# Performance work log

Measured on AMD Instinct MI355X. Metric: run time of the kernel, lower is better.

Reference implementation:

```python
import jax, jax.numpy as jnp
import numpy as np

B, T = 64, 20          # batch, caption length
C, HW = 512, 196       # cnn_channels, width*height (14x14)
V, E, U = 10000, 256, 512  # n_tokens, emb_size, lstm_units
MAX_NORM = 5.0


def setup_inputs() -> dict:
    key = jax.random.key(0)
    ks = jax.random.split(key, 12)
    s = 0.02
    return {
        "image_features": jax.random.normal(ks[0], (B, C, HW), jnp.float32),
        "captions_ix": jax.random.randint(ks[1], (B, T), 0, V, dtype=jnp.int32),
        "W_h0": jax.random.normal(ks[2], (U, C), jnp.float32) * s,
        "b_h0": jnp.zeros((U,), jnp.float32),
        "W_c0": jax.random.normal(ks[3], (U, C), jnp.float32) * s,
        "b_c0": jnp.zeros((U,), jnp.float32),
        "emb": jax.random.normal(ks[4], (V, E), jnp.float32) * s,
        "W_key": jax.random.normal(ks[5], (U, C), jnp.float32) * s,
        "b_key": jnp.zeros((U,), jnp.float32),
        "W_ih": jax.random.normal(ks[6], (4 * U, C + E), jnp.float32) * s,
        "b_ih": jnp.zeros((4 * U,), jnp.float32),
        "W_hh": jax.random.normal(ks[7], (4 * U, U), jnp.float32) * s,
        "b_hh": jnp.zeros((4 * U,), jnp.float32),
        "W_out": jax.random.normal(ks[8], (V, C + E + U), jnp.float32) * s,
        "b_out": jnp.zeros((V,), jnp.float32),
    }


def _caption_net(image_features, captions_ix, W_h0, b_h0, W_c0, b_c0, emb,
                 W_key, b_key, W_ih, b_ih, W_hh, b_hh, W_out, b_out):
    feats_mean = image_features.mean(axis=2)                # [B, C]
    hid0 = feats_mean @ W_h0.T + b_h0                       # [B, U]
    cell0 = feats_mean @ W_c0.T + b_c0                      # [B, U]
    feats = jnp.transpose(image_features, (0, 2, 1))        # [B, HW, C]
    keys = feats @ W_key.T + b_key                          # [B, HW, U]

    # nn.Embedding(max_norm=5): renorm rows whose L2 norm exceeds 5
    norms = jnp.linalg.norm(emb, axis=1, keepdims=True)
    emb_eff = emb * jnp.minimum(1.0, MAX_NORM / jnp.maximum(norms, 1e-12))
    cap_emb = emb_eff[captions_ix]                          # [B, T, E]

    inv_scale = 1.0 / (keys.shape[2] ** 0.5)

    def step(carry, emb_t):
        hid, cell = carry
        # scaled dot-product attention, query = current hidden state
        scores = jnp.einsum('bu,bku->bk', hid, keys) * inv_scale   # [B, HW]
        w = jax.nn.softmax(scores, axis=1)
        a = jnp.einsum('bk,bkc->bc', w, feats)                     # [B, C]
        x = jnp.concatenate([emb_t, a], axis=1)                    # [B, E+C]
        gates = x @ W_ih.T + b_ih + hid @ W_hh.T + b_hh            # [B, 4U]
        i, f, g, o = jnp.split(gates, 4, axis=1)
        cell = jax.nn.sigmoid(f) * cell + jax.nn.sigmoid(i) * jnp.tanh(g)
        hid = jax.nn.sigmoid(o) * jnp.tanh(cell)
        out = jnp.concatenate([hid, a, emb_t], axis=1)             # [B, U+C+E]
        return (hid, cell), (out, w)

    (_, _), (outs, attn) = jax.lax.scan(step, (hid0, cell0),
                                        jnp.transpose(cap_emb, (1, 0, 2)))
    outs = jnp.transpose(outs, (1, 0, 2))                   # [B, T, U+C+E]
    attn = jnp.transpose(attn, (1, 0, 2))                   # [B, T, HW]
    logits = outs @ W_out.T + b_out                         # [B, T, V]
    return logits, attn


def reference(image_features, captions_ix, W_h0, b_h0, W_c0, b_c0, emb,
              W_key, b_key, W_ih, b_ih, W_hh, b_hh, W_out, b_out):
    return _caption_net(image_features, captions_ix, W_h0, b_h0, W_c0, b_c0,
                        emb, W_key, b_key, W_ih, b_ih, W_hh, b_hh, W_out, b_out)
```

## Files before the change

kernel.cpp:

```cpp
#include <hip/hip_runtime.h>
#include <math.h>

#define B 64
#define T 20
#define C 512
#define HW 196
#define V 10000
#define E 256
#define U 512
#define G4U 2048
#define ODIM 1280
#define KTOT 1280

typedef short bf8_t __attribute__((ext_vector_type(8)));
typedef float f4_t  __attribute__((ext_vector_type(4)));

__device__ __forceinline__ unsigned short f2bf(float f) {
    unsigned int u = __float_as_uint(f);
    return (unsigned short)((u + 0x7fffu + ((u >> 16) & 1u)) >> 16);
}
__device__ __forceinline__ float bf2f(unsigned short s) {
    return __uint_as_float((unsigned int)s << 16);
}
__device__ __forceinline__ float bflo(unsigned int kv) { return __uint_as_float(kv << 16); }
__device__ __forceinline__ float bfhi(unsigned int kv) { return __uint_as_float(kv & 0xffff0000u); }

__global__ void k_mean(const float* __restrict__ img, float* __restrict__ fm) {
    int wave = threadIdx.x >> 6;
    int lane = threadIdx.x & 63;
    int row = blockIdx.x * 4 + wave;
    const float* p = img + (size_t)row * HW;
    float s = p[lane] + p[lane + 64] + p[lane + 128];
    if (lane < 4) s += p[lane + 192];
    for (int off = 32; off > 0; off >>= 1) s += __shfl_down(s, off, 64);
    if (lane == 0) fm[row] = s * (1.0f / HW);
}

__global__ void k_init(const float* __restrict__ fm,
                       const float* __restrict__ W_h0, const float* __restrict__ b_h0,
                       const float* __restrict__ W_c0, const float* __restrict__ b_c0,
                       unsigned short* __restrict__ xb, float* __restrict__ cell) {
    int wv = blockIdx.x * 4 + (threadIdx.x >> 6);
    int lane = threadIdx.x & 63;
    int which = wv >> 15;
    int r = wv & 32767;
    int b = r >> 9, u = r & 511;
    const float* W = which ? W_c0 : W_h0;
    const float* bias = which ? b_c0 : b_h0;
    const float* f = fm + b * C;
    const float* w = W + (size_t)u * C;
    float s = 0.f;
    #pragma unroll
    for (int c = 0; c < C; c += 64) s += f[c + lane] * w[c + lane];
    for (int off = 32; off > 0; off >>= 1) s += __shfl_down(s, off, 64);
    if (lane == 0) {
        float v = s + bias[u];
        if (which) cell[r] = v;
        else       xb[(size_t)b * KTOT + 768 + u] = f2bf(v);
    }
}

__global__ void k_wkt(const float* __restrict__ Wk, float* __restrict__ WkT) {
    __shared__ float tile[64][65];
    int u0 = blockIdx.x * 64, c0 = blockIdx.y * 64;
    int x = threadIdx.x & 63, y0 = threadIdx.x >> 6;
    #pragma unroll
    for (int i = 0; i < 16; i++) {
        int r = y0 * 16 + i;
        tile[r][x] = Wk[(size_t)(u0 + r) * C + c0 + x];
    }
    __syncthreads();
    #pragma unroll
    for (int i = 0; i < 16; i++) {
        int r = y0 * 16 + i;
        WkT[(size_t)(c0 + r) * U + u0 + x] = tile[x][r];
    }
}

__global__ __launch_bounds__(256) void k_keys(const float* __restrict__ img,
        const float* __restrict__ WkT, const float* __restrict__ b_key,
        unsigned short* __restrict__ keys2) {
    __shared__ unsigned short st[32][200];
    int b = blockIdx.x >> 4;
    int u0 = (blockIdx.x & 15) * 32;
    int wave = __builtin_amdgcn_readfirstlane(threadIdx.x >> 6);
    int lane = threadIdx.x & 63;
    int lk = lane < 49 ? lane : 48;
    const f4_t* imgb = (const f4_t*)(img + (size_t)b * C * HW);
    f4_t acc[8];
    #pragma unroll
    for (int j = 0; j < 8; j++) acc[j] = (f4_t){0.f, 0.f, 0.f, 0.f};
    const float* wp = WkT + u0 + wave * 8;
    for (int c = 0; c < C; c++) {
        f4_t v = imgb[c * 49 + lk];
        const float* w = wp + (size_t)c * U;
        #pragma unroll
        for (int j = 0; j < 8; j++) acc[j] += v * w[j];
    }
    if (lane < 49) {
        #pragma unroll
        for (int j = 0; j < 8; j++) {
            float bk = b_key[u0 + wave * 8 + j];
            int ul = wave * 8 + j;
            int k = lane * 4;
            st[ul][k + 0] = f2bf(acc[j].x + bk);
            st[ul][k + 1] = f2bf(acc[j].y + bk);
            st[ul][k + 2] = f2bf(acc[j].z + bk);
            st[ul][k + 3] = f2bf(acc[j].w + bk);
        }
    }
    __syncthreads();
    int ui = threadIdx.x & 15;
    int kr = threadIdx.x >> 4;
    #pragma unroll
    for (int pass = 0; pass < 13; pass++) {
        int k = pass * 16 + kr;
        if (k < HW) {
            unsigned int lo = st[ui * 2][k];
            unsigned int hi = st[ui * 2 + 1][k];
            *(unsigned int*)&keys2[((size_t)b * HW + k) * U + u0 + ui * 2] = (hi << 16) | lo;
        }
    }
}

__global__ void k_wg(const float* __restrict__ W_ih, const float* __restrict__ W_hh,
                     unsigned short* __restrict__ Wg) {
    int j = blockIdx.x;
    int tid = threadIdx.x;
    const float* s1 = W_ih + (size_t)j * 768;
    const float* s2 = W_hh + (size_t)j * 512;
    unsigned short* dst = Wg + (size_t)j * KTOT;
    #pragma unroll
    for (int p = 0; p < 3; p++) dst[tid + p * 256] = f2bf(s1[tid + p * 256]);
    #pragma unroll
    for (int p = 0; p < 2; p++) dst[768 + tid + p * 256] = f2bf(s2[tid + p * 256]);
}

__global__ void k_emb(const int* __restrict__ ix, const float* __restrict__ emb,
                      unsigned short* __restrict__ outs) {
    int bt = blockIdx.x;
    int e = threadIdx.x;
    int row = ix[bt];
    float v = emb[(size_t)row * E + e];
    __shared__ float red[4];
    float sq = v * v;
    for (int off = 32; off > 0; off >>= 1) sq += __shfl_down(sq, off, 64);
    int wave = e >> 6, lane = e & 63;
    if (lane == 0) red[wave] = sq;
    __syncthreads();
    float norm = sqrtf(red[0] + red[1] + red[2] + red[3]);
    float scale = fminf(1.0f, 5.0f / fmaxf(norm, 1e-12f));
    outs[(size_t)bt * ODIM + (U + C) + e] = f2bf(v * scale);
}

__global__ __launch_bounds__(256) void k_step(
    unsigned short* __restrict__ outs, unsigned short* __restrict__ xb,
    float* __restrict__ cell, const float* __restrict__ gates_buf,
    const unsigned short* __restrict__ keys2, const float* __restrict__ img,
    const float* __restrict__ b_ih, const float* __restrict__ b_hh,
    float* __restrict__ attn, int t) {
    int b = blockIdx.x;
    int tid = threadIdx.x;
    int wave = tid >> 6, lane = tid & 63;
    __shared__ float hidS[U];
    __shared__ float wS[256];
    __shared__ float red[4];

    if (t > 0) {
        #pragma unroll
        for (int p = 0; p < 2; p++) {
            int u = tid + p * 256;
            float g[4];
            #pragma unroll
            for (int q = 0; q < 4; q++) {
                int j = q * 512 + u;
                g[q] = gates_buf[(size_t)b * G4U + j] + b_ih[j] + b_hh[j];
            }
            float si = 1.f / (1.f + expf(-g[0]));
            float sf = 1.f / (1.f + expf(-g[1]));
            float tg = tanhf(g[2]);
            float so = 1.f / (1.f + expf(-g[3]));
            int ci = b * U + u;
            float cn = sf * cell[ci] + si * tg;
            float hn = so * tanhf(cn);
            cell[ci] = cn;
            hidS[u] = hn;
            outs[((size_t)b * T + (t - 1)) * ODIM + u] = f2bf(hn);
            xb[(size_t)b * KTOT + 768 + u] = f2bf(hn);
        }
    } else {
        #pragma unroll
        for (int p = 0; p < 2; p++) {
            int u = tid + p * 256;
            hidS[u] = bf2f(xb[(size_t)b * KTOT + 768 + u]);
        }
    }
    if (t >= T) return;
    __syncthreads();

    float sc = 0.f;
    if (tid < HW) {
        const uint4* kr = (const uint4*)(keys2 + ((size_t)b * HW + tid) * U);
        float acc = 0.f;
        #pragma unroll 8
        for (int i = 0; i < 64; i++) {
            uint4 kv = kr[i];
            float4 h0 = *(const float4*)&hidS[i * 8];
            float4 h1 = *(const float4*)&hidS[i * 8 + 4];
            acc += bflo(kv.x) * h0.x + bfhi(kv.x) * h0.y
                 + bflo(kv.y) * h0.z + bfhi(kv.y) * h0.w
                 + bflo(kv.z) * h1.x + bfhi(kv.z) * h1.y
                 + bflo(kv.w) * h1.z + bfhi(kv.w) * h1.w;
        }
        sc = acc * 0.044194173824159216f;
    }
    {
        float v = (tid < HW) ? sc : -1e30f;
        float m = v;
        for (int off = 32; off > 0; off >>= 1) m = fmaxf(m, __shfl_down(m, off, 64));
        if (lane == 0) red[wave] = m;
        __syncthreads();
        m = fmaxf(fmaxf(red[0], red[1]), fmaxf(red[2], red[3]));
        float ex = (tid < HW) ? expf(v - m) : 0.f;
        float ssum = ex;
        for (int off = 32; off > 0; off >>= 1) ssum += __shfl_down(ssum, off, 64);
        __syncthreads();
        if (lane == 0) red[wave] = ssum;
        __syncthreads();
        ssum = red[0] + red[1] + red[2] + red[3];
        float w = ex / ssum;
        wS[tid] = w;
        if (tid < HW) attn[((size_t)b * T + t) * HW + tid] = w;
    }
    __syncthreads();

    {
        const float4* imgb = (const float4*)(img + (size_t)b * C * HW);
        #pragma unroll
        for (int p = 0; p < 2; p++) {
            int c = tid + p * 256;
            const float4* r = imgb + c * 49;
            float acc = 0.f;
            for (int k4 = 0; k4 < 49; k4++) {
                float4 vv = r[k4];
                acc += wS[4 * k4] * vv.x + wS[4 * k4 + 1] * vv.y
                     + wS[4 * k4 + 2] * vv.z + wS[4 * k4 + 3] * vv.w;
            }
            xb[(size_t)b * KTOT + 256 + c] = f2bf(acc);
            outs[((size_t)b * T + t) * ODIM + U + c] = f2bf(acc);
        }
    }
    if (tid < 128) {
        const unsigned int* src = (const unsigned int*)(outs + ((size_t)b * T + t) * ODIM);
        unsigned int* dst = (unsigned int*)(xb + (size_t)b * KTOT);
        dst[tid] = src[512 + tid];
    }
}

__global__ __launch_bounds__(256) void k_gates5(
    const unsigned short* __restrict__ xb, const unsigned short* __restrict__ Wg,
    float* __restrict__ gates_buf) {
    __shared__ unsigned short As[64][72];
    __shared__ unsigned short Bs[64][72];
    int j0 = blockIdx.x * 64;
    int tid = threadIdx.x;
    int lane = tid & 63;
    int wv = __builtin_amdgcn_readfirstlane(tid >> 6);
    int m16 = lane & 15, quad = lane >> 4;
    int r = tid >> 2;
    int kq = tid & 3;

    f4_t acc[4];
    #pragma unroll
    for (int i = 0; i < 4; i++) acc[i] = (f4_t){0.f, 0.f, 0.f, 0.f};

    for (int k0 = 0; k0 < KTOT; k0 += 64) {
        const uint4* ap = (const uint4*)&xb[(size_t)r * KTOT + k0 + kq * 16];
        uint4 a0 = ap[0], a1 = ap[1];
        const uint4* bp = (const uint4*)&Wg[(size_t)(j0 + r) * KTOT + k0 + kq * 16];
        uint4 b0 = bp[0], b1 = bp[1];
        *(uint4*)&As[r][kq * 16] = a0;
        *(uint4*)&As[r][kq * 16 + 8] = a1;
        *(uint4*)&Bs[r][kq * 16] = b0;
        *(uint4*)&Bs[r][kq * 16 + 8] = b1;
        __syncthreads();
        #pragma unroll
        for (int h = 0; h < 2; h++) {
            bf8_t bfr = *(const bf8_t*)&Bs[wv * 16 + m16][h * 32 + quad * 8];
            #pragma unroll
            for (int i = 0; i < 4; i++) {
                bf8_t afr = *(const bf8_t*)&As[i * 16 + m16][h * 32 + quad * 8];
                acc[i] = __builtin_amdgcn_mfma_f32_16x16x32_bf16(afr, bfr, acc[i], 0, 0, 0);
            }
        }
        __syncthreads();
    }
    int n = j0 + wv * 16 + m16;
    #pragma unroll
    for (int i = 0; i < 4; i++) {
        int mb = i * 16 + quad * 4;
        #pragma unroll
        for (int rr = 0; rr < 4; rr++)
            gates_buf[(size_t)(mb + rr) * G4U + n] = acc[i][rr];
    }
}

__global__ __launch_bounds__(256) void k_logits4(
    const unsigned short* __restrict__ A, const float* __restrict__ Wo,
    const float* __restrict__ bo, float* __restrict__ Cout) {
    __shared__ unsigned short As[128][72];
    __shared__ unsigned short Bs[128][72];
    int n0 = blockIdx.x * 128;
    int m0 = blockIdx.y * 128;
    int tid = threadIdx.x;
    int lane = tid & 63, wv = tid >> 6;
    int mw = (wv >> 1) * 64, nw = (wv & 1) * 64;
    int m16 = lane & 15, quad = lane >> 4;
    int srow = tid >> 1, shalf = tid & 1;

    f4_t acc[4][4];
    #pragma unroll
    for (int i = 0; i < 4; i++)
        #pragma unroll
        for (int j = 0; j < 4; j++)
            acc[i][j] = (f4_t){0.f, 0.f, 0.f, 0.f};

    for (int k0 = 0; k0 < KTOT; k0 += 64) {
        {
            const uint4* ap = (const uint4*)&A[(size_t)(m0 + srow) * KTOT + k0 + shalf * 32];
            uint4 a0 = ap[0], a1 = ap[1], a2 = ap[2], a3 = ap[3];
            uint4* dst = (uint4*)&As[srow][shalf * 32];
            dst[0] = a0; dst[1] = a1; dst[2] = a2; dst[3] = a3;
        }
        {
            int n = n0 + srow;
            uint4 q[4];
            if (n < V) {
                const float4* bp = (const float4*)&Wo[(size_t)n * KTOT + k0 + shalf * 32];
                #pragma unroll
                for (int g = 0; g < 4; g++) {
                    float4 f0 = bp[g * 2], f1 = bp[g * 2 + 1];
                    q[g].x = ((unsigned int)f2bf(f0.y) << 16) | f2bf(f0.x);
                    q[g].y = ((unsigned int)f2bf(f0.w) << 16) | f2bf(f0.z);
                    q[g].z = ((unsigned int)f2bf(f1.y) << 16) | f2bf(f1.x);
                    q[g].w = ((unsigned int)f2bf(f1.w) << 16) | f2bf(f1.z);
                }
            } else {
                #pragma unroll
                for (int g = 0; g < 4; g++) q[g] = (uint4){0u, 0u, 0u, 0u};
            }
            uint4* dst = (uint4*)&Bs[srow][shalf * 32];
            #pragma unroll
            for (int g = 0; g < 4; g++) dst[g] = q[g];
        }
        __syncthreads();
        #pragma unroll
        for (int h = 0; h < 2; h++) {
            bf8_t af[4], bf[4];
            #pragma unroll
            for (int i = 0; i < 4; i++)
                af[i] = *(const bf8_t*)&As[mw + i * 16 + m16][h * 32 + quad * 8];
            #pragma unroll
            for (int j = 0; j < 4; j++)
                bf[j] = *(const bf8_t*)&Bs[nw + j * 16 + m16][h * 32 + quad * 8];
            #pragma unroll
            for (int i = 0; i < 4; i++)
                #pragma unroll
                for (int j = 0; j < 4; j++)
                    acc[i][j] = __builtin_amdgcn_mfma_f32_16x16x32_bf16(af[i], bf[j], acc[i][j], 0, 0, 0);
        }
        __syncthreads();
    }

    #pragma unroll
    for (int j = 0; j < 4; j++) {
        int n = n0 + nw + j * 16 + m16;
        if (n >= V) continue;
        float bias = bo[n];
        #pragma unroll
        for (int i = 0; i < 4; i++) {
            int mb = m0 + mw + i * 16 + quad * 4;
            #pragma unroll
            for (int r = 0; r < 4; r++)
                Cout[(size_t)(mb + r) * V + n] = acc[i][j][r] + bias;
        }
    }
}

extern "C" void kernel_launch(void* const* d_in, const int* in_sizes, int n_in,
                              void* d_out, int out_size, void* d_ws, size_t ws_size,
                              hipStream_t stream) {
    const float* img   = (const float*)d_in[0];
    const int*   capix = (const int*)d_in[1];
    const float* W_h0  = (const float*)d_in[2];
    const float* b_h0  = (const float*)d_in[3];
    const float* W_c0  = (const float*)d_in[4];
    const float* b_c0  = (const float*)d_in[5];
    const float* emb   = (const float*)d_in[6];
    const float* W_key = (const float*)d_in[7];
    const float* b_key = (const float*)d_in[8];
    const float* W_ih  = (const float*)d_in[9];
    const float* b_ih  = (const float*)d_in[10];
    const float* W_hh  = (const float*)d_in[11];
    const float* b_hh  = (const float*)d_in[12];
    const float* W_out = (const float*)d_in[13];
    const float* b_out = (const float*)d_in[14];

    float* ws = (float*)d_ws;
    float* gates_buf = ws;
    float* fm        = ws;
    float* cell      = gates_buf + 131072;
    float* WkT       = cell + 32768;
    unsigned short* Wg    = (unsigned short*)(WkT + 262144);
    unsigned short* xb    = Wg + 2621440;
    unsigned short* outs  = xb + 81920;
    unsigned short* keys2 = outs + (size_t)B * T * ODIM;

    float* logits = (float*)d_out;
    float* attn   = logits + (size_t)B * T * V;

    k_mean<<<(B * C) / 4, 256, 0, stream>>>(img, fm);
    k_init<<<(2 * B * U) / 4, 256, 0, stream>>>(fm, W_h0, b_h0, W_c0, b_c0, xb, cell);
    k_wkt<<<dim3(8, 8), 256, 0, stream>>>(W_key, WkT);
    k_keys<<<B * 16, 256, 0, stream>>>(img, WkT, b_key, keys2);
    k_wg<<<G4U, 256, 0, stream>>>(W_ih, W_hh, Wg);
    k_emb<<<B * T, 256, 0, stream>>>(capix, emb, outs);

    for (int t = 0; t < T; t++) {
        k_step<<<B, 256, 0, stream>>>(outs, xb, cell, gates_buf, keys2, img,
                                      b_ih, b_hh, attn, t);
        k_gates5<<<32, 256, 0, stream>>>(xb, Wg, gates_buf);
    }
    k_step<<<B, 256, 0, stream>>>(outs, xb, cell, gates_buf, keys2, img,
                                  b_ih, b_hh, attn, T);

    k_logits4<<<dim3((V + 127) / 128, (B * T) / 128), 256, 0, stream>>>(outs, W_out, b_out, logits);
}
```

Baseline: 1.381 ms.

## Fuse recurrent loop into one persistent kernel with grid barriers; pre-convert W_out

Replaces the 41 per-timestep launches (step + gates GEMM) with one persistent 64-block kernel that alternates attention/LSTM work and a split gates GEMM, separated by atomic-counter grid barriers; the cell state and bias sums are held in registers. It also adds a prefetching double-load in the gates GEMM and a separate pass converting W_out to bf16 once so the logits GEMM loads bf16 directly. This removes launch overhead and redundant fp32->bf16 conversion, at the risk of spin-barrier cost and co-residency assumptions for the 64 blocks.

```diff
diff --git a/kernel.cpp b/kernel.cpp
--- a/kernel.cpp
+++ b/kernel.cpp
@@ -11,6 +11,7 @@
 #define G4U 2048
 #define ODIM 1280
 #define KTOT 1280
+#define NBLK 64
 
 typedef short bf8_t __attribute__((ext_vector_type(8)));
 typedef float f4_t  __attribute__((ext_vector_type(4)));
@@ -25,7 +26,26 @@
 __device__ __forceinline__ float bflo(unsigned int kv) { return __uint_as_float(kv << 16); }
 __device__ __forceinline__ float bfhi(unsigned int kv) { return __uint_as_float(kv & 0xffff0000u); }
 
-__global__ void k_mean(const float* __restrict__ img, float* __restrict__ fm) {
+__device__ __forceinline__ void gbar(int* bar) {
+    __syncthreads();
+    if (threadIdx.x == 0) {
+        __threadfence();
+        int g = __hip_atomic_load(bar + 1, __ATOMIC_RELAXED, __HIP_MEMORY_SCOPE_AGENT);
+        if (__hip_atomic_fetch_add(bar, 1, __ATOMIC_RELAXED, __HIP_MEMORY_SCOPE_AGENT) == NBLK - 1) {
+            __hip_atomic_store(bar, 0, __ATOMIC_RELAXED, __HIP_MEMORY_SCOPE_AGENT);
+            __hip_atomic_store(bar + 1, g + 1, __ATOMIC_RELEASE, __HIP_MEMORY_SCOPE_AGENT);
+        } else {
+            while (__hip_atomic_load(bar + 1, __ATOMIC_RELAXED, __HIP_MEMORY_SCOPE_AGENT) == g)
+                __builtin_amdgcn_s_sleep(1);
+        }
+        __threadfence();
+    }
+    __syncthreads();
+}
+
+__global__ void k_mean(const float* __restrict__ img, float* __restrict__ fm,
+                       int* __restrict__ bar) {
+    if (blockIdx.x == 0 && threadIdx.x == 0) { bar[0] = 0; bar[1] = 0; }
     int wave = threadIdx.x >> 6;
     int lane = threadIdx.x & 63;
     int row = blockIdx.x * 4 + wave;
@@ -153,155 +173,181 @@
     outs[(size_t)bt * ODIM + (U + C) + e] = f2bf(v * scale);
 }
 
-__global__ __launch_bounds__(256) void k_step(
+__global__ __launch_bounds__(256) void k_wo(const float* __restrict__ W,
+                                            unsigned short* __restrict__ Wb) {
+    size_t i = ((size_t)blockIdx.x * 256 + threadIdx.x) * 8;
+    float4 f0 = *(const float4*)(W + i);
+    float4 f1 = *(const float4*)(W + i + 4);
+    uint4 q;
+    q.x = ((unsigned int)f2bf(f0.y) << 16) | f2bf(f0.x);
+    q.y = ((unsigned int)f2bf(f0.w) << 16) | f2bf(f0.z);
+    q.z = ((unsigned int)f2bf(f1.y) << 16) | f2bf(f1.x);
+    q.w = ((unsigned int)f2bf(f1.w) << 16) | f2bf(f1.z);
+    *(uint4*)(Wb + i) = q;
+}
+
+__global__ __launch_bounds__(256) void k_loop(
     unsigned short* __restrict__ outs, unsigned short* __restrict__ xb,
-    float* __restrict__ cell, const float* __restrict__ gates_buf,
+    const float* __restrict__ cell0, float* __restrict__ gates_buf,
     const unsigned short* __restrict__ keys2, const float* __restrict__ img,
     const float* __restrict__ b_ih, const float* __restrict__ b_hh,
-    float* __restrict__ attn, int t) {
+    const unsigned short* __restrict__ Wg, float* __restrict__ attn,
+    int* __restrict__ bar) {
     int b = blockIdx.x;
     int tid = threadIdx.x;
-    int wave = tid >> 6, lane = tid & 63;
+    int wave = __builtin_amdgcn_readfirstlane(tid >> 6);
+    int lane = tid & 63;
+    int m16 = lane & 15, quad = lane >> 4;
     __shared__ float hidS[U];
     __shared__ float wS[256];
     __shared__ float red[4];
-
-    if (t > 0) {
-        #pragma unroll
-        for (int p = 0; p < 2; p++) {
-            int u = tid + p * 256;
-            float g[4];
-            #pragma unroll
-            for (int q = 0; q < 4; q++) {
-                int j = q * 512 + u;
-                g[q] = gates_buf[(size_t)b * G4U + j] + b_ih[j] + b_hh[j];
-            }
-            float si = 1.f / (1.f + expf(-g[0]));
-            float sf = 1.f / (1.f + expf(-g[1]));
-            float tg = tanhf(g[2]);
-            float so = 1.f / (1.f + expf(-g[3]));
-            int ci = b * U + u;
-            float cn = sf * cell[ci] + si * tg;
-            float hn = so * tanhf(cn);
-            cell[ci] = cn;
-            hidS[u] = hn;
-            outs[((size_t)b * T + (t - 1)) * ODIM + u] = f2bf(hn);
-            xb[(size_t)b * KTOT + 768 + u] = f2bf(hn);
-        }
-    } else {
-        #pragma unroll
-        for (int p = 0; p < 2; p++) {
-            int u = tid + p * 256;
-            hidS[u] = bf2f(xb[(size_t)b * KTOT + 768 + u]);
-        }
-    }
-    if (t >= T) return;
-    __syncthreads();
-
-    float sc = 0.f;
-    if (tid < HW) {
-        const uint4* kr = (const uint4*)(keys2 + ((size_t)b * HW + tid) * U);
-        float acc = 0.f;
-        #pragma unroll 8
-        for (int i = 0; i < 64; i++) {
-            uint4 kv = kr[i];
-            float4 h0 = *(const float4*)&hidS[i * 8];
-            float4 h1 = *(const float4*)&hidS[i * 8 + 4];
-            acc += bflo(kv.x) * h0.x + bfhi(kv.x) * h0.y
-                 + bflo(kv.y) * h0.z + bfhi(kv.y) * h0.w
-                 + bflo(kv.z) * h1.x + bfhi(kv.z) * h1.y
-                 + bflo(kv.w) * h1.z + bfhi(kv.w) * h1.w;
-        }
-        sc = acc * 0.044194173824159216f;
-    }
-    {
-        float v = (tid < HW) ? sc : -1e30f;
-        float m = v;
-        for (int off = 32; off > 0; off >>= 1) m = fmaxf(m, __shfl_down(m, off, 64));
-        if (lane == 0) red[wave] = m;
+    __shared__ unsigned short As2[64][72];
+    __shared__ unsigned short Bs2[32][72];
+
+    float c_r[2], bsum[2][4];
+    #pragma unroll
+    for (int p = 0; p < 2; p++) {
+        int u = tid + p * 256;
+        c_r[p] = cell0[(size_t)b * U + u];
+        #pragma unroll
+        for (int q = 0; q < 4; q++)
+            bsum[p][q] = b_ih[q * 512 + u] + b_hh[q * 512 + u];
+    }
+
+    int j0g = blockIdx.x * 32;
+    int r = tid >> 2, kq = tid & 3;
+    int rb = tid >> 3, kb = tid & 7;
+    int n16 = wave & 1, mpair = wave >> 1;
+
+    for (int t = 0; t <= T; ++t) {
+        if (t > 0) {
+            #pragma unroll
+            for (int p = 0; p < 2; p++) {
+                int u = tid + p * 256;
+                float g[4];
+                #pragma unroll
+                for (int q = 0; q < 4; q++)
+                    g[q] = gates_buf[(size_t)b * G4U + q * 512 + u] + bsum[p][q];
+                float si = 1.f / (1.f + expf(-g[0]));
+                float sf = 1.f / (1.f + expf(-g[1]));
+                float tg = tanhf(g[2]);
+                float so = 1.f / (1.f + expf(-g[3]));
+                float cn = sf * c_r[p] + si * tg;
+                c_r[p] = cn;
+                float hn = so * tanhf(cn);
+                hidS[u] = hn;
+                outs[((size_t)b * T + (t - 1)) * ODIM + u] = f2bf(hn);
+                xb[(size_t)b * KTOT + 768 + u] = f2bf(hn);
+            }
+        } else {
+            #pragma unroll
+            for (int p = 0; p < 2; p++) {
+                int u = tid + p * 256;
+                hidS[u] = bf2f(xb[(size_t)b * KTOT + 768 + u]);
+            }
+        }
+        if (t == T) break;
         __syncthreads();
-        m = fmaxf(fmaxf(red[0], red[1]), fmaxf(red[2], red[3]));
-        float ex = (tid < HW) ? expf(v - m) : 0.f;
-        float ssum = ex;
-        for (int off = 32; off > 0; off >>= 1) ssum += __shfl_down(ssum, off, 64);
+
+        float sc = 0.f;
+        if (tid < HW) {
+            const uint4* kr = (const uint4*)(keys2 + ((size_t)b * HW + tid) * U);
+            float acc = 0.f;
+            #pragma unroll 8
+            for (int i = 0; i < 64; i++) {
+                uint4 kv = kr[i];
+                float4 h0 = *(const float4*)&hidS[i * 8];
+                float4 h1 = *(const float4*)&hidS[i * 8 + 4];
+                acc += bflo(kv.x) * h0.x + bfhi(kv.x) * h0.y
+                     + bflo(kv.y) * h0.z + bfhi(kv.y) * h0.w
+                     + bflo(kv.z) * h1.x + bfhi(kv.z) * h1.y
+                     + bflo(kv.w) * h1.z + bfhi(kv.w) * h1.w;
+            }
+            sc = acc * 0.044194173824159216f;
+        }
+        {
+            float v = (tid < HW) ? sc : -1e30f;
+            float m = v;
+            for (int off = 32; off > 0; off >>= 1) m = fmaxf(m, __shfl_down(m, off, 64));
+            if (lane == 0) red[wave] = m;
+            __syncthreads();
+            m = fmaxf(fmaxf(red[0], red[1]), fmaxf(red[2], red[3]));
+            float ex = (tid < HW) ? expf(v - m) : 0.f;
+            float ssum = ex;
+            for (int off = 32; off > 0; off >>= 1) ssum += __shfl_down(ssum, off, 64);
+            __syncthreads();
+            if (lane == 0) red[wave] = ssum;
+            __syncthreads();
+            ssum = red[0] + red[1] + red[2] + red[3];
+            float w = ex / ssum;
+            wS[tid] = w;
+            if (tid < HW) attn[((size_t)b * T + t) * HW + tid] = w;
+        }
         __syncthreads();
-        if (lane == 0) red[wave] = ssum;
-        __syncthreads();
-        ssum = red[0] + red[1] + red[2] + red[3];
-        float w = ex / ssum;
-        wS[tid] = w;
-        if (tid < HW) attn[((size_t)b * T + t) * HW + tid] = w;
-    }
-    __syncthreads();
-
-    {
-        const float4* imgb = (const float4*)(img + (size_t)b * C * HW);
-        #pragma unroll
-        for (int p = 0; p < 2; p++) {
-            int c = tid + p * 256;
-            const float4* r = imgb + c * 49;
-            float acc = 0.f;
-            for (int k4 = 0; k4 < 49; k4++) {
-                float4 vv = r[k4];
-                acc += wS[4 * k4] * vv.x + wS[4 * k4 + 1] * vv.y
-                     + wS[4 * k4 + 2] * vv.z + wS[4 * k4 + 3] * vv.w;
-            }
-            xb[(size_t)b * KTOT + 256 + c] = f2bf(acc);
-            outs[((size_t)b * T + t) * ODIM + U + c] = f2bf(acc);
-        }
-    }
-    if (tid < 128) {
-        const unsigned int* src = (const unsigned int*)(outs + ((size_t)b * T + t) * ODIM);
-        unsigned int* dst = (unsigned int*)(xb + (size_t)b * KTOT);
-        dst[tid] = src[512 + tid];
-    }
-}
-
-__global__ __launch_bounds__(256) void k_gates5(
-    const unsigned short* __restrict__ xb, const unsigned short* __restrict__ Wg,
-    float* __restrict__ gates_buf) {
-    __shared__ unsigned short As[64][72];
-    __shared__ unsigned short Bs[64][72];
-    int j0 = blockIdx.x * 64;
-    int tid = threadIdx.x;
-    int lane = tid & 63;
-    int wv = __builtin_amdgcn_readfirstlane(tid >> 6);
-    int m16 = lane & 15, quad = lane >> 4;
-    int r = tid >> 2;
-    int kq = tid & 3;
-
-    f4_t acc[4];
-    #pragma unroll
-    for (int i = 0; i < 4; i++) acc[i] = (f4_t){0.f, 0.f, 0.f, 0.f};
-
-    for (int k0 = 0; k0 < KTOT; k0 += 64) {
-        const uint4* ap = (const uint4*)&xb[(size_t)r * KTOT + k0 + kq * 16];
-        uint4 a0 = ap[0], a1 = ap[1];
-        const uint4* bp = (const uint4*)&Wg[(size_t)(j0 + r) * KTOT + k0 + kq * 16];
-        uint4 b0 = bp[0], b1 = bp[1];
-        *(uint4*)&As[r][kq * 16] = a0;
-        *(uint4*)&As[r][kq * 16 + 8] = a1;
-        *(uint4*)&Bs[r][kq * 16] = b0;
-        *(uint4*)&Bs[r][kq * 16 + 8] = b1;
-        __syncthreads();
-        #pragma unroll
-        for (int h = 0; h < 2; h++) {
-            bf8_t bfr = *(const bf8_t*)&Bs[wv * 16 + m16][h * 32 + quad * 8];
-            #pragma unroll
-            for (int i = 0; i < 4; i++) {
-                bf8_t afr = *(const bf8_t*)&As[i * 16 + m16][h * 32 + quad * 8];
-                acc[i] = __builtin_amdgcn_mfma_f32_16x16x32_bf16(afr, bfr, acc[i], 0, 0, 0);
-            }
-        }
-        __syncthreads();
-    }
-    int n = j0 + wv * 16 + m16;
-    #pragma unroll
-    for (int i = 0; i < 4; i++) {
-        int mb = i * 16 + quad * 4;
-        #pragma unroll
-        for (int rr = 0; rr < 4; rr++)
-            gates_buf[(size_t)(mb + rr) * G4U + n] = acc[i][rr];
+
+        {
+            const float4* imgb = (const float4*)(img + (size_t)b * C * HW);
+            #pragma unroll
+            for (int p = 0; p < 2; p++) {
+                int c = tid + p * 256;
+                const float4* rr4 = imgb + c * 49;
+                float acc = 0.f;
+                for (int k4 = 0; k4 < 49; k4++) {
+                    float4 vv = rr4[k4];
+                    acc += wS[4 * k4] * vv.x + wS[4 * k4 + 1] * vv.y
+                         + wS[4 * k4 + 2] * vv.z + wS[4 * k4 + 3] * vv.w;
+                }
+                xb[(size_t)b * KTOT + 256 + c] = f2bf(acc);
+                outs[((size_t)b * T + t) * ODIM + U + c] = f2bf(acc);
+            }
+        }
+        if (tid < 128) {
+            const unsigned int* src = (const unsigned int*)(outs + ((size_t)b * T + t) * ODIM);
+            unsigned int* dst = (unsigned int*)(xb + (size_t)b * KTOT);
+            dst[tid] = src[512 + tid];
+        }
+
+        gbar(bar);
+
+        {
+            f4_t acc2[2];
+            acc2[0] = (f4_t){0.f, 0.f, 0.f, 0.f};
+            acc2[1] = (f4_t){0.f, 0.f, 0.f, 0.f};
+            const uint4* ap0 = (const uint4*)&xb[(size_t)r * KTOT + kq * 16];
+            uint4 a0 = ap0[0], a1 = ap0[1];
+            uint4 bq = *(const uint4*)&Wg[(size_t)(j0g + rb) * KTOT + kb * 8];
+            for (int k0 = 0; k0 < KTOT; k0 += 64) {
+                *(uint4*)&As2[r][kq * 16]     = a0;
+                *(uint4*)&As2[r][kq * 16 + 8] = a1;
+                *(uint4*)&Bs2[rb][kb * 8]     = bq;
+                __syncthreads();
+                if (k0 + 64 < KTOT) {
+                    const uint4* apn = (const uint4*)&xb[(size_t)r * KTOT + k0 + 64 + kq * 16];
+                    a0 = apn[0]; a1 = apn[1];
+                    bq = *(const uint4*)&Wg[(size_t)(j0g + rb) * KTOT + k0 + 64 + kb * 8];
+                }
+                #pragma unroll
+                for (int h = 0; h < 2; h++) {
+                    bf8_t bfr = *(const bf8_t*)&Bs2[n16 * 16 + m16][h * 32 + quad * 8];
+                    #pragma unroll
+                    for (int i2 = 0; i2 < 2; i2++) {
+                        bf8_t afr = *(const bf8_t*)&As2[(mpair * 2 + i2) * 16 + m16][h * 32 + quad * 8];
+                        acc2[i2] = __builtin_amdgcn_mfma_f32_16x16x32_bf16(afr, bfr, acc2[i2], 0, 0, 0);
+                    }
+                }
+                __syncthreads();
+            }
+            int n = j0g + n16 * 16 + m16;
+            #pragma unroll
+            for (int i2 = 0; i2 < 2; i2++) {
+                int mb = (mpair * 2 + i2) * 16 + quad * 4;
+                #pragma unroll
+                for (int rr = 0; rr < 4; rr++)
+                    gates_buf[(size_t)(mb + rr) * G4U + n] = acc2[i2][rr];
+            }
+        }
+
+        gbar(bar);
     }
 }
 
@@ -345,6 +391,82 @@
                     q[g].z = ((unsigned int)f2bf(f1.y) << 16) | f2bf(f1.x);
                     q[g].w = ((unsigned int)f2bf(f1.w) << 16) | f2bf(f1.z);
                 }
+            } else {
+                #pragma unroll
+                for (int g = 0; g < 4; g++) q[g] = (uint4){0u, 0u, 0u, 0u};
+            }
+            uint4* dst = (uint4*)&Bs[srow][shalf * 32];
+            #pragma unroll
+            for (int g = 0; g < 4; g++) dst[g] = q[g];
+        }
+        __syncthreads();
+        #pragma unroll
+        for (int h = 0; h < 2; h++) {
+            bf8_t af[4], bf[4];
+            #pragma unroll
+            for (int i = 0; i < 4; i++)
+                af[i] = *(const bf8_t*)&As[mw + i * 16 + m16][h * 32 + quad * 8];
+            #pragma unroll
+            for (int j = 0; j < 4; j++)
+                bf[j] = *(const bf8_t*)&Bs[nw + j * 16 + m16][h * 32 + quad * 8];
+            #pragma unroll
+            for (int i = 0; i < 4; i++)
+                #pragma unroll
+                for (int j = 0; j < 4; j++)
+                    acc[i][j] = __builtin_amdgcn_mfma_f32_16x16x32_bf16(af[i], bf[j], acc[i][j], 0, 0, 0);
+        }
+        __syncthreads();
+    }
+
+    #pragma unroll
+    for (int j = 0; j < 4; j++) {
+        int n = n0 + nw + j * 16 + m16;
+        if (n >= V) continue;
+        float bias = bo[n];
+        #pragma unroll
+        for (int i = 0; i < 4; i++) {
+            int mb = m0 + mw + i * 16 + quad * 4;
+            #pragma unroll
+            for (int r = 0; r < 4; r++)
+                Cout[(size_t)(mb + r) * V + n] = acc[i][j][r] + bias;
+        }
+    }
+}
+
+__global__ __launch_bounds__(256) void k_logits5(
+    const unsigned short* __restrict__ A, const unsigned short* __restrict__ Wob,
+    const float* __restrict__ bo, float* __restrict__ Cout) {
+    __shared__ unsigned short As[128][72];
+    __shared__ unsigned short Bs[128][72];
+    int n0 = blockIdx.x * 128;
+    int m0 = blockIdx.y * 128;
+    int tid = threadIdx.x;
+    int lane = tid & 63, wv = tid >> 6;
+    int mw = (wv >> 1) * 64, nw = (wv & 1) * 64;
+    int m16 = lane & 15, quad = lane >> 4;
+    int srow = tid >> 1, shalf = tid & 1;
+
+    f4_t acc[4][4];
+    #pragma unroll
+    for (int i = 0; i < 4; i++)
+        #pragma unroll
+        for (int j = 0; j < 4; j++)
+            acc[i][j] = (f4_t){0.f, 0.f, 0.f, 0.f};
+
+    for (int k0 = 0; k0 < KTOT; k0 += 64) {
+        {
+            const uint4* ap = (const uint4*)&A[(size_t)(m0 + srow) * KTOT + k0 + shalf * 32];
+            uint4 a0 = ap[0], a1 = ap[1], a2 = ap[2], a3 = ap[3];
+            uint4* dst = (uint4*)&As[srow][shalf * 32];
+            dst[0] = a0; dst[1] = a1; dst[2] = a2; dst[3] = a3;
+        }
+        {
+            int n = n0 + srow;
+            uint4 q[4];
+            if (n < V) {
+                const uint4* bp = (const uint4*)&Wob[(size_t)n * KTOT + k0 + shalf * 32];
+                #pragma unroll
+                for (int g = 0; g < 4; g++) q[g] = bp[g];
             } else {
                 #pragma unroll
                 for (int g = 0; g < 4; g++) q[g] = (uint4){0u, 0u, 0u, 0u};
@@ -415,24 +537,28 @@
     unsigned short* xb    = Wg + 2621440;
     unsigned short* outs  = xb + 81920;
     unsigned short* keys2 = outs + (size_t)B * T * ODIM;
+    int* bar = (int*)(keys2 + (size_t)B * HW * U);
+    const size_t WOB_OFF = 23232576;
+    unsigned short* Wob = (unsigned short*)((char*)d_ws + WOB_OFF);
+    bool use_wob = ws_size >= WOB_OFF + (size_t)V * KTOT * 2;
 
     float* logits = (float*)d_out;
     float* attn   = logits + (size_t)B * T * V;
 
-    k_mean<<<(B * C) / 4, 256, 0, stream>>>(img, fm);
+    k_mean<<<(B * C) / 4, 256, 0, stream>>>(img, fm, bar);
     k_init<<<(2 * B * U) / 4, 256, 0, stream>>>(fm, W_h0, b_h0, W_c0, b_c0, xb, cell);
     k_wkt<<<dim3(8, 8), 256, 0, stream>>>(W_key, WkT);
     k_keys<<<B * 16, 256, 0, stream>>>(img, WkT, b_key, keys2);
     k_wg<<<G4U, 256, 0, stream>>>(W_ih, W_hh, Wg);
     k_emb<<<B * T, 256, 0, stream>>>(capix, emb, outs);
-
-    for (int t = 0; t < T; t++) {
-        k_step<<<B, 256, 0, stream>>>(outs, xb, cell, gates_buf, keys2, img,
-                                      b_ih, b_hh, attn, t);
-        k_gates5<<<32, 256, 0, stream>>>(xb, Wg, gates_buf);
-    }
-    k_step<<<B, 256, 0, stream>>>(outs, xb, cell, gates_buf, keys2, img,
-                                  b_ih, b_hh, attn, T);
-
-    k_logits4<<<dim3((V + 127) / 128, (B * T) / 128), 256, 0, stream>>>(outs, W_out, b_out, logits);
-}
+    if (use_wob)
+        k_wo<<<(V * KTOT) / 2048, 256, 0, stream>>>(W_out, Wob);
+
+    k_loop<<<NBLK, 256, 0, stream>>>(outs, xb, cell, gates_buf, keys2, img,
+                                     b_ih, b_hh, Wg, attn, bar);
+
+    if (use_wob)
+        k_logits5<<<dim3((V + 127) / 128, (B * T) / 128), 256, 0, stream>>>(outs, Wob, b_out, logits);
+    else
+        k_logits4<<<dim3((V + 127) / 128, (B * T) / 128), 256, 0, stream>>>(outs, W_out, b_out, logits);
+}
```

New measurement: 1.438 ms. 1.04x slower.
